# Kernel optimization log

Hardware: AMD Instinct MI355X
Metric: run time of the kernel (lower is better)

## Reference

```python
import jax, jax.numpy as jnp
import numpy as np

WINDOW = 10


def setup_inputs() -> dict:
    key = jax.random.key(0)
    k_r, k_w1, k_b1, k_w2, k_b2 = jax.random.split(key, 5)
    B, T = 2048, 4096
    returns = jax.random.normal(k_r, (B, T), dtype=jnp.float32)
    # nn.Linear default init ~ U(-1/sqrt(fan_in), 1/sqrt(fan_in)); scaled normals are fine for a reference
    W1 = jax.random.normal(k_w1, (32, WINDOW), dtype=jnp.float32) / np.sqrt(WINDOW)
    b1 = jax.random.normal(k_b1, (32,), dtype=jnp.float32) * 0.01
    W2 = jax.random.normal(k_w2, (1, 32), dtype=jnp.float32) / np.sqrt(32)
    b2 = jax.random.normal(k_b2, (1,), dtype=jnp.float32) * 0.01
    return {"returns": returns, "W1": W1, "b1": b1, "W2": W2, "b2": b2}


def reference(returns, W1, b1, W2, b2) -> jnp.ndarray:
    B, T = returns.shape
    w = WINDOW
    # Gather all sliding windows at once: window i covers returns[:, i:i+w] and
    # produces the estimate for timestep t = i + w (matching the torch loop).
    idx = jnp.arange(T - w)[:, None] + jnp.arange(w)[None, :]  # [T-w, w]
    wins = returns[:, idx]  # [B, T-w, w]
    h1 = jax.nn.relu(jnp.einsum('btw,hw->bth', wins, W1) + b1)  # [B, T-w, 32]
    h = 0.5 * jax.nn.sigmoid(jnp.einsum('bth,oh->bto', h1, W2) + b2)[..., 0]  # [B, T-w]
    # H[:, :window] = H[:, window] (the first computed value)
    head = jnp.broadcast_to(h[:, :1], (B, w))
    return jnp.concatenate([head, h], axis=1)  # [B, T]
```

## Files before the change

kernel.cpp:

```cpp
#include <hip/hip_runtime.h>

#define WINDOW 10
#define TDIM 4096
#define TVALID (TDIM - WINDOW)

typedef __attribute__((ext_vector_type(8)))  short bf16x8;
typedef __attribute__((ext_vector_type(8)))  __bf16 bfv8;
typedef __attribute__((ext_vector_type(8)))  float f32x8;
typedef __attribute__((ext_vector_type(16))) float f32x16;
typedef __attribute__((ext_vector_type(2)))  float f32x2;
typedef float f32x4u __attribute__((ext_vector_type(4), aligned(4)));

static __device__ __forceinline__ short f2bf(float f) {
  return (short)__builtin_bit_cast(unsigned short, (__bf16)f);
}

static __device__ __forceinline__ f32x8 ld8(const float* __restrict__ p) {
  f32x4u a = *(const f32x4u*)p;
  f32x4u b = *(const f32x4u*)(p + 4);
  f32x8 f;
  f[0] = a[0]; f[1] = a[1]; f[2] = a[2]; f[3] = a[3];
  f[4] = b[0]; f[5] = b[1]; f[6] = b[2]; f[7] = b[3];
  return f;
}

static __device__ __forceinline__ f32x8 ld8c(const float* __restrict__ rowp, int base) {
  f32x8 f;
  #pragma unroll
  for (int j = 0; j < 8; ++j) {
    int idx = base + j; idx = idx < TDIM - 1 ? idx : TDIM - 1;
    f[j] = rowp[idx];
  }
  return f;
}

static __device__ __forceinline__ bf16x8 packbf(f32x8 f, bool g1) {
  f[2] = g1 ? 1.0f : f[2];
  return __builtin_bit_cast(bf16x8, __builtin_convertvector(f, bfv8));
}

static __device__ __forceinline__ float l2dot(const f32x16& acc, const f32x2* __restrict__ w2p) {
  const f32x2 z2 = {0.f, 0.f};
  f32x2 s0 = z2, s1 = z2;
  #pragma unroll
  for (int j = 0; j < 8; j += 2) {
    f32x2 a = {acc[2*j],     acc[2*j + 1]};
    f32x2 b = {acc[2*j + 2], acc[2*j + 3]};
    s0 = __builtin_elementwise_fma(__builtin_elementwise_max(a, z2), w2p[j],     s0);
    s1 = __builtin_elementwise_fma(__builtin_elementwise_max(b, z2), w2p[j + 1], s1);
  }
  f32x2 s = s0 + s1;
  return s[0] + s[1];
}

static __device__ __forceinline__ float combine_halves(float Pe, float Po, int lid) {
#if __has_builtin(__builtin_amdgcn_permlane32_swap)
  auto r = __builtin_amdgcn_permlane32_swap(
      __builtin_bit_cast(unsigned, Pe), __builtin_bit_cast(unsigned, Po), false, false);
  return __builtin_bit_cast(float, (unsigned)r[0]) + __builtin_bit_cast(float, (unsigned)r[1]);
#else
  Pe += __shfl_xor(Pe, 32, 64);
  Po += __shfl_xor(Po, 32, 64);
  return (lid < 32) ? Pe : Po;
#endif
}

static __device__ __forceinline__ float half_sigmoid(float z) {
  float e = __expf(-z);
#if __has_builtin(__builtin_amdgcn_rcpf)
  return 0.5f * __builtin_amdgcn_rcpf(1.0f + e);
#else
  return 0.5f / (1.0f + e);
#endif
}

__global__ __launch_bounds__(256) void hurst_mfma5(
    const float* __restrict__ ret, const float* __restrict__ W1,
    const float* __restrict__ b1,  const float* __restrict__ W2,
    const float* __restrict__ b2,  float* __restrict__ out) {
  const int lid = threadIdx.x & 63;
  const int wv  = threadIdx.x >> 6;
  const int n   = lid & 31;
  const int g   = lid >> 5;
  const bool g1 = (g == 1);

  bf16x8 af;
  if (!g1) {
    #pragma unroll
    for (int j = 0; j < 8; ++j) af[j] = f2bf(W1[n * WINDOW + j]);
  } else {
    af[0] = f2bf(W1[n * WINDOW + 8]);
    af[1] = f2bf(W1[n * WINDOW + 9]);
    af[2] = f2bf(b1[n]);
    #pragma unroll
    for (int j = 3; j < 8; ++j) af[j] = 0;
  }

  f32x2 w2p[8];
  #pragma unroll
  for (int j = 0; j < 8; ++j) {
    w2p[j][0] = W2[((2*j)   & 3) + 8 * ((2*j)   >> 2) + 4 * g];
    w2p[j][1] = W2[((2*j+1) & 3) + 8 * ((2*j+1) >> 2) + 4 * g];
  }
  const float b2c = b2[0];

  const int row = blockIdx.x;
  const float* __restrict__ rowp = ret + (size_t)row * TDIM;
  float* __restrict__ orow = out + (size_t)row * TDIM;
  const int seg   = wv * 1024;
  const int lbase = n + 8 * g;
  const float* __restrict__ lanep = rowp + seg + lbase;

  f32x8 fe = ld8(lanep);
  f32x8 fo = ld8(lanep + 32);
  float y;

#define PAIR(P, PRE, MASK)                                                     \
  {                                                                            \
    bf16x8 bve = packbf(fe, g1);                                               \
    f32x16 acce = {};                                                          \
    acce = __builtin_amdgcn_mfma_f32_32x32x16_bf16(af, bve, acce, 0, 0, 0);    \
    if (PRE) fe = ld8(lanep + (2*(P)+2) * 32);                                 \
    float Pe = l2dot(acce, w2p);                                               \
    bf16x8 bvo = packbf(fo, g1);                                               \
    f32x16 acco = {};                                                          \
    acco = __builtin_amdgcn_mfma_f32_32x32x16_bf16(af, bvo, acco, 0, 0, 0);    \
    if (PRE) fo = ld8(lanep + (2*(P)+3) * 32);                                 \
    float Po = l2dot(acco, w2p);                                               \
    const float q = combine_halves(Pe, Po, lid);                               \
    y = half_sigmoid(q + b2c);                                                 \
    const int t = seg + (P) * 64 + lid;                                        \
    if (!(MASK) || t < TVALID) orow[WINDOW + t] = y;                           \
  }

  PAIR(0, true, false)
  if (wv == 0) {
    const float y0 = __shfl(y, 0, 64);
    if (lid < WINDOW) orow[lid] = y0;
  }

  #pragma unroll
  for (int p = 1; p <= 13; ++p) PAIR(p, true, false)

  {
    bf16x8 bve = packbf(fe, g1);
    f32x16 acce = {};
    acce = __builtin_amdgcn_mfma_f32_32x32x16_bf16(af, bve, acce, 0, 0, 0);
    fe = ld8(lanep + 30 * 32);
    float Pe = l2dot(acce, w2p);
    bf16x8 bvo = packbf(fo, g1);
    f32x16 acco = {};
    acco = __builtin_amdgcn_mfma_f32_32x32x16_bf16(af, bvo, acco, 0, 0, 0);
    if (wv == 3) fo = ld8c(rowp, seg + 31 * 32 + lbase);
    else         fo = ld8(lanep + 31 * 32);
    float Po = l2dot(acco, w2p);
    const float q = combine_halves(Pe, Po, lid);
    y = half_sigmoid(q + b2c);
    orow[WINDOW + seg + 14 * 64 + lid] = y;
  }

  PAIR(15, false, true)
#undef PAIR
}

extern "C" void kernel_launch(void* const* d_in, const int* in_sizes, int n_in,
                              void* d_out, int out_size, void* d_ws, size_t ws_size,
                              hipStream_t stream) {
  const float* ret = (const float*)d_in[0];
  const float* W1  = (const float*)d_in[1];
  const float* b1  = (const float*)d_in[2];
  const float* W2  = (const float*)d_in[3];
  const float* b2  = (const float*)d_in[4];
  float* out = (float*)d_out;

  const int B = in_sizes[0] / TDIM;
  dim3 block(256);
  dim3 grid(B);
  hipLaunchKernelGGL(hurst_mfma5, grid, block, 0, stream,
                     ret, W1, b1, W2, b2, out);
}
```

Measured before the change: 44.98 us.

## Pre-convert input rows to bf16 in a workspace staging kernel before MFMA pass

Adds a prestage kernel that converts each fp32 input row to bf16, padding with the last value, into a workspace. The main kernel then reads the bf16 rows, and the bias-slot substitution is done with integer masks rather than per-element conversion. The f32 path is kept as a fallback when the workspace is too small. This removes conversion work and halves the bytes read by the MFMA kernel. The cost is an extra launch plus a full fp32 read and bf16 write/read round trip, and the main kernel no longer software-pipelines its loads.

```diff
diff --git a/kernel.cpp b/kernel.cpp
--- a/kernel.cpp
+++ b/kernel.cpp
@@ -3,51 +3,30 @@
 #define WINDOW 10
 #define TDIM 4096
 #define TVALID (TDIM - WINDOW)
+#define WSTRIDE 4160
 
 typedef __attribute__((ext_vector_type(8)))  short bf16x8;
 typedef __attribute__((ext_vector_type(8)))  __bf16 bfv8;
 typedef __attribute__((ext_vector_type(8)))  float f32x8;
 typedef __attribute__((ext_vector_type(16))) float f32x16;
 typedef __attribute__((ext_vector_type(2)))  float f32x2;
+typedef __attribute__((ext_vector_type(4)))  unsigned u32x4;
 typedef float f32x4u __attribute__((ext_vector_type(4), aligned(4)));
+typedef short s16x8u __attribute__((ext_vector_type(8), aligned(2)));
 
 static __device__ __forceinline__ short f2bf(float f) {
   return (short)__builtin_bit_cast(unsigned short, (__bf16)f);
 }
 
-static __device__ __forceinline__ f32x8 ld8(const float* __restrict__ p) {
-  f32x4u a = *(const f32x4u*)p;
-  f32x4u b = *(const f32x4u*)(p + 4);
-  f32x8 f;
-  f[0] = a[0]; f[1] = a[1]; f[2] = a[2]; f[3] = a[3];
-  f[4] = b[0]; f[5] = b[1]; f[6] = b[2]; f[7] = b[3];
-  return f;
-}
-
-static __device__ __forceinline__ f32x8 ld8c(const float* __restrict__ rowp, int base) {
-  f32x8 f;
-  #pragma unroll
-  for (int j = 0; j < 8; ++j) {
-    int idx = base + j; idx = idx < TDIM - 1 ? idx : TDIM - 1;
-    f[j] = rowp[idx];
-  }
-  return f;
-}
-
-static __device__ __forceinline__ bf16x8 packbf(f32x8 f, bool g1) {
-  f[2] = g1 ? 1.0f : f[2];
-  return __builtin_bit_cast(bf16x8, __builtin_convertvector(f, bfv8));
-}
-
 static __device__ __forceinline__ float l2dot(const f32x16& acc, const f32x2* __restrict__ w2p) {
-  const f32x2 z2 = {0.f, 0.f};
-  f32x2 s0 = z2, s1 = z2;
+  f32x2 s0 = {0.f, 0.f}, s1 = {0.f, 0.f};
   #pragma unroll
   for (int j = 0; j < 8; j += 2) {
-    f32x2 a = {acc[2*j],     acc[2*j + 1]};
-    f32x2 b = {acc[2*j + 2], acc[2*j + 3]};
-    s0 = __builtin_elementwise_fma(__builtin_elementwise_max(a, z2), w2p[j],     s0);
-    s1 = __builtin_elementwise_fma(__builtin_elementwise_max(b, z2), w2p[j + 1], s1);
+    f32x2 a, b;
+    a[0] = fmaxf(acc[2*j],     0.f); a[1] = fmaxf(acc[2*j + 1], 0.f);
+    b[0] = fmaxf(acc[2*j + 2], 0.f); b[1] = fmaxf(acc[2*j + 3], 0.f);
+    s0 = __builtin_elementwise_fma(a, w2p[j],     s0);
+    s1 = __builtin_elementwise_fma(b, w2p[j + 1], s1);
   }
   f32x2 s = s0 + s1;
   return s[0] + s[1];
@@ -74,93 +53,158 @@
 #endif
 }
 
-__global__ __launch_bounds__(256) void hurst_mfma5(
+__global__ __launch_bounds__(256) void prestage(const float* __restrict__ ret,
+                                                unsigned short* __restrict__ ws) {
+  const int row = blockIdx.x;
+  const float* __restrict__ rowp = ret + (size_t)row * TDIM;
+  unsigned short* __restrict__ wrow = ws + (size_t)row * WSTRIDE;
+  const float last = rowp[TDIM - 1];
+  for (int c = threadIdx.x; c < WSTRIDE / 8; c += 256) {
+    f32x8 f;
+    if (c < TDIM / 8) {
+      f32x4u a = *(const f32x4u*)(rowp + 8 * c);
+      f32x4u b = *(const f32x4u*)(rowp + 8 * c + 4);
+      f[0]=a[0]; f[1]=a[1]; f[2]=a[2]; f[3]=a[3];
+      f[4]=b[0]; f[5]=b[1]; f[6]=b[2]; f[7]=b[3];
+    } else {
+      for (int j = 0; j < 8; ++j) f[j] = last;
+    }
+    bfv8 h = __builtin_convertvector(f, bfv8);
+    *(bf16x8*)(wrow + 8 * c) = __builtin_bit_cast(bf16x8, h);
+  }
+}
+
+struct Setup {
+  bf16x8 af; f32x2 w2p[8]; float b2c;
+  int lid, n, g; bool g1;
+};
+static __device__ __forceinline__ Setup make_setup(
+    const float* __restrict__ W1, const float* __restrict__ b1,
+    const float* __restrict__ W2, const float* __restrict__ b2) {
+  Setup s;
+  s.lid = threadIdx.x & 63; s.n = s.lid & 31; s.g = s.lid >> 5; s.g1 = (s.g == 1);
+  if (!s.g1) {
+    #pragma unroll
+    for (int j = 0; j < 8; ++j) s.af[j] = f2bf(W1[s.n * WINDOW + j]);
+  } else {
+    s.af[0] = f2bf(W1[s.n * WINDOW + 8]);
+    s.af[1] = f2bf(W1[s.n * WINDOW + 9]);
+    s.af[2] = f2bf(b1[s.n]);
+    #pragma unroll
+    for (int j = 3; j < 8; ++j) s.af[j] = 0;
+  }
+  #pragma unroll
+  for (int j = 0; j < 8; ++j) {
+    s.w2p[j][0] = W2[((2*j)   & 3) + 8 * ((2*j)   >> 2) + 4 * s.g];
+    s.w2p[j][1] = W2[((2*j+1) & 3) + 8 * ((2*j+1) >> 2) + 4 * s.g];
+  }
+  s.b2c = b2[0];
+  return s;
+}
+
+static __device__ __forceinline__ float pair_bf(
+    const Setup& S, const unsigned short* __restrict__ lanep, int p,
+    unsigned andm, unsigned orm) {
+  s16x8u ve = *(const s16x8u*)(lanep + p * 64);
+  s16x8u vo = *(const s16x8u*)(lanep + p * 64 + 32);
+  u32x4 ue = __builtin_bit_cast(u32x4, ve);
+  u32x4 uo = __builtin_bit_cast(u32x4, vo);
+  ue[1] = (ue[1] & andm) | orm;
+  uo[1] = (uo[1] & andm) | orm;
+  f32x16 acce = {}, acco = {};
+  acce = __builtin_amdgcn_mfma_f32_32x32x16_bf16(S.af, __builtin_bit_cast(bf16x8, ue), acce, 0, 0, 0);
+  acco = __builtin_amdgcn_mfma_f32_32x32x16_bf16(S.af, __builtin_bit_cast(bf16x8, uo), acco, 0, 0, 0);
+  float Pe = l2dot(acce, S.w2p);
+  float Po = l2dot(acco, S.w2p);
+  const float q = combine_halves(Pe, Po, S.lid);
+  return half_sigmoid(q + S.b2c);
+}
+
+__global__ __launch_bounds__(256) void hurst_main_bf(
+    const unsigned short* __restrict__ ws, const float* __restrict__ W1,
+    const float* __restrict__ b1,  const float* __restrict__ W2,
+    const float* __restrict__ b2,  float* __restrict__ out) {
+  Setup S = make_setup(W1, b1, W2, b2);
+  const int wv  = threadIdx.x >> 6;
+  const int row = blockIdx.x;
+  const int seg = wv * 1024;
+  const unsigned andm = S.g1 ? 0xFFFF0000u : 0xFFFFFFFFu;
+  const unsigned orm  = S.g1 ? 0x00003F80u : 0u;
+
+  const unsigned short* __restrict__ lanep = ws + (size_t)row * WSTRIDE + seg + S.n + 8 * S.g;
+  float* __restrict__ orow = out + (size_t)row * TDIM;
+
+  float y = pair_bf(S, lanep, 0, andm, orm);
+  orow[WINDOW + seg + S.lid] = y;
+  if (wv == 0) {
+    const float y0 = __shfl(y, 0, 64);
+    if (S.lid < WINDOW) orow[S.lid] = y0;
+  }
+  #pragma unroll
+  for (int p = 1; p < 15; ++p) {
+    y = pair_bf(S, lanep, p, andm, orm);
+    orow[WINDOW + seg + p * 64 + S.lid] = y;
+  }
+  y = pair_bf(S, lanep, 15, andm, orm);
+  const int t = seg + 15 * 64 + S.lid;
+  if (t < TVALID) orow[WINDOW + t] = y;
+}
+
+static __device__ __forceinline__ f32x8 ld8(const float* __restrict__ p) {
+  f32x4u a = *(const f32x4u*)p;
+  f32x4u b = *(const f32x4u*)(p + 4);
+  f32x8 f; f[0]=a[0];f[1]=a[1];f[2]=a[2];f[3]=a[3];f[4]=b[0];f[5]=b[1];f[6]=b[2];f[7]=b[3];
+  return f;
+}
+static __device__ __forceinline__ bf16x8 packbf(f32x8 f, bool g1) {
+  f[2] = g1 ? 1.0f : f[2];
+  return __builtin_bit_cast(bf16x8, __builtin_convertvector(f, bfv8));
+}
+static __device__ __forceinline__ float pair_f32(
+    const Setup& S, const float* __restrict__ rowp, int seg, int p, bool clamp) {
+  const int lbase = S.n + 8 * S.g;
+  f32x8 fe = ld8(rowp + seg + p * 64 + lbase);
+  f32x8 fo;
+  if (clamp) {
+    for (int j = 0; j < 8; ++j) {
+      int idx = seg + p * 64 + 32 + lbase + j;
+      idx = idx < TDIM - 1 ? idx : TDIM - 1;
+      fo[j] = rowp[idx];
+    }
+  } else {
+    fo = ld8(rowp + seg + p * 64 + 32 + lbase);
+  }
+  bf16x8 bve = packbf(fe, S.g1), bvo = packbf(fo, S.g1);
+  f32x16 acce = {}, acco = {};
+  acce = __builtin_amdgcn_mfma_f32_32x32x16_bf16(S.af, bve, acce, 0, 0, 0);
+  acco = __builtin_amdgcn_mfma_f32_32x32x16_bf16(S.af, bvo, acco, 0, 0, 0);
+  float Pe = l2dot(acce, S.w2p);
+  float Po = l2dot(acco, S.w2p);
+  const float q = combine_halves(Pe, Po, S.lid);
+  return half_sigmoid(q + S.b2c);
+}
+__global__ __launch_bounds__(256) void hurst_main_f32(
     const float* __restrict__ ret, const float* __restrict__ W1,
     const float* __restrict__ b1,  const float* __restrict__ W2,
     const float* __restrict__ b2,  float* __restrict__ out) {
-  const int lid = threadIdx.x & 63;
+  Setup S = make_setup(W1, b1, W2, b2);
   const int wv  = threadIdx.x >> 6;
-  const int n   = lid & 31;
-  const int g   = lid >> 5;
-  const bool g1 = (g == 1);
-
-  bf16x8 af;
-  if (!g1) {
-    #pragma unroll
-    for (int j = 0; j < 8; ++j) af[j] = f2bf(W1[n * WINDOW + j]);
-  } else {
-    af[0] = f2bf(W1[n * WINDOW + 8]);
-    af[1] = f2bf(W1[n * WINDOW + 9]);
-    af[2] = f2bf(b1[n]);
-    #pragma unroll
-    for (int j = 3; j < 8; ++j) af[j] = 0;
-  }
-
-  f32x2 w2p[8];
-  #pragma unroll
-  for (int j = 0; j < 8; ++j) {
-    w2p[j][0] = W2[((2*j)   & 3) + 8 * ((2*j)   >> 2) + 4 * g];
-    w2p[j][1] = W2[((2*j+1) & 3) + 8 * ((2*j+1) >> 2) + 4 * g];
-  }
-  const float b2c = b2[0];
-
   const int row = blockIdx.x;
+  const int seg = wv * 1024;
   const float* __restrict__ rowp = ret + (size_t)row * TDIM;
   float* __restrict__ orow = out + (size_t)row * TDIM;
-  const int seg   = wv * 1024;
-  const int lbase = n + 8 * g;
-  const float* __restrict__ lanep = rowp + seg + lbase;
-
-  f32x8 fe = ld8(lanep);
-  f32x8 fo = ld8(lanep + 32);
-  float y;
-
-#define PAIR(P, PRE, MASK)                                                     \
-  {                                                                            \
-    bf16x8 bve = packbf(fe, g1);                                               \
-    f32x16 acce = {};                                                          \
-    acce = __builtin_amdgcn_mfma_f32_32x32x16_bf16(af, bve, acce, 0, 0, 0);    \
-    if (PRE) fe = ld8(lanep + (2*(P)+2) * 32);                                 \
-    float Pe = l2dot(acce, w2p);                                               \
-    bf16x8 bvo = packbf(fo, g1);                                               \
-    f32x16 acco = {};                                                          \
-    acco = __builtin_amdgcn_mfma_f32_32x32x16_bf16(af, bvo, acco, 0, 0, 0);    \
-    if (PRE) fo = ld8(lanep + (2*(P)+3) * 32);                                 \
-    float Po = l2dot(acco, w2p);                                               \
-    const float q = combine_halves(Pe, Po, lid);                               \
-    y = half_sigmoid(q + b2c);                                                 \
-    const int t = seg + (P) * 64 + lid;                                        \
-    if (!(MASK) || t < TVALID) orow[WINDOW + t] = y;                           \
-  }
-
-  PAIR(0, true, false)
-  if (wv == 0) {
-    const float y0 = __shfl(y, 0, 64);
-    if (lid < WINDOW) orow[lid] = y0;
-  }
-
-  #pragma unroll
-  for (int p = 1; p <= 13; ++p) PAIR(p, true, false)
-
-  {
-    bf16x8 bve = packbf(fe, g1);
-    f32x16 acce = {};
-    acce = __builtin_amdgcn_mfma_f32_32x32x16_bf16(af, bve, acce, 0, 0, 0);
-    fe = ld8(lanep + 30 * 32);
-    float Pe = l2dot(acce, w2p);
-    bf16x8 bvo = packbf(fo, g1);
-    f32x16 acco = {};
-    acco = __builtin_amdgcn_mfma_f32_32x32x16_bf16(af, bvo, acco, 0, 0, 0);
-    if (wv == 3) fo = ld8c(rowp, seg + 31 * 32 + lbase);
-    else         fo = ld8(lanep + 31 * 32);
-    float Po = l2dot(acco, w2p);
-    const float q = combine_halves(Pe, Po, lid);
-    y = half_sigmoid(q + b2c);
-    orow[WINDOW + seg + 14 * 64 + lid] = y;
-  }
-
-  PAIR(15, false, true)
-#undef PAIR
+
+  float y = pair_f32(S, rowp, seg, 0, false);
+  orow[WINDOW + seg + S.lid] = y;
+  if (wv == 0) { const float y0 = __shfl(y, 0, 64); if (S.lid < WINDOW) orow[S.lid] = y0; }
+  #pragma unroll
+  for (int p = 1; p < 15; ++p) {
+    y = pair_f32(S, rowp, seg, p, false);
+    orow[WINDOW + seg + p * 64 + S.lid] = y;
+  }
+  y = pair_f32(S, rowp, seg, 15, wv == 3);
+  const int t = seg + 15 * 64 + S.lid;
+  if (t < TVALID) orow[WINDOW + t] = y;
 }
 
 extern "C" void kernel_launch(void* const* d_in, const int* in_sizes, int n_in,
@@ -174,8 +218,16 @@
   float* out = (float*)d_out;
 
   const int B = in_sizes[0] / TDIM;
+  const size_t need = (size_t)B * WSTRIDE * sizeof(unsigned short);
   dim3 block(256);
   dim3 grid(B);
-  hipLaunchKernelGGL(hurst_mfma5, grid, block, 0, stream,
-                     ret, W1, b1, W2, b2, out);
-}
+  if (ws_size >= need) {
+    unsigned short* ws = (unsigned short*)d_ws;
+    hipLaunchKernelGGL(prestage, grid, block, 0, stream, ret, ws);
+    hipLaunchKernelGGL(hurst_main_bf, grid, block, 0, stream,
+                       ws, W1, b1, W2, b2, out);
+  } else {
+    hipLaunchKernelGGL(hurst_main_f32, grid, block, 0, stream,
+                       ret, W1, b1, W2, b2, out);
+  }
+}
```

Measured after the change: 54.83 us. 1.22x slower.
